# Optimization experiments

Hardware: AMD Instinct MI355X
Metric: run time of the kernel (lower is better)

The kernel has to match this reference:

```python
import jax, jax.numpy as jnp
import numpy as np

B, C, HS, WS = 4, 256, 64, 64
NK, NV, NH = 32, 32, 8
QKV = NK * NV + NK + NV  # 1088


def setup_inputs() -> dict:
    key = jax.random.key(0)
    k1, k2, k3, k4 = jax.random.split(key, 4)
    x = jax.random.normal(k1, (B, C, HS, WS), dtype=jnp.float32)
    Wqkv = jax.random.normal(k2, (NH, QKV, C), dtype=jnp.float32) * (C ** -0.5)
    Wc = jax.random.normal(k3, (C, NV * NH), dtype=jnp.float32) * ((NV * NH) ** -0.5)
    bc = jax.random.normal(k4, (C,), dtype=jnp.float32) * 0.01
    return {"x": x, "Wqkv": Wqkv, "Wc": Wc, "bc": bc}


def reference(x, Wqkv, Wc, bc):
    b, c, h, w = x.shape
    n = h * w
    xt = x.reshape(b, c, n).transpose(0, 2, 1)  # (B, N, C)
    # All heads' QKV projections in one einsum (torch loops over heads)
    qkv = jnp.einsum('bnc,hqc->bhnq', xt, Wqkv)  # (B, NH, N, QKV)
    q = qkv[..., :NK]                                            # (B,NH,N,NK)
    k = qkv[..., NK:NK + NK * NV].reshape(b, NH, n, NK, NV)      # (B,NH,N,NK,NV)
    v = qkv[..., NK + NK * NV:]                                  # (B,NH,N,NV)
    # per-pixel tiny matmul: (1xNK) @ (NKxNV) -> NV, scaled
    qk = jnp.einsum('bhnk,bhnkv->bhnv', q, k) / (NK ** 0.5)
    a = jax.nn.softmax(qk, axis=-1) * v  # (B, NH, N, NV)
    # concat heads along channel dim (head-major), then combine Linear
    a = a.transpose(0, 2, 1, 3).reshape(b, n, NH * NV)  # (B, N, NH*NV)
    out = a @ Wc.T + bc  # (B, N, C)
    return out.transpose(0, 2, 1).reshape(b, c, h, w)
```

## Files before the change

### kernel.cpp

```cpp
#include <hip/hip_runtime.h>

#define NPIX_TOTAL 16384
#define CDIM 256
#define NHEADS 8
#define QKVD 1088
#define NQKV 8704

typedef unsigned short u16;
typedef __attribute__((ext_vector_type(8))) __bf16 bf16x8;
typedef __attribute__((ext_vector_type(4))) float f32x4;
typedef __attribute__((ext_vector_type(2))) unsigned u32x2;

__device__ static inline u16 f2bf(float f) {
  union { float f; unsigned u; } x; x.f = f;
  unsigned r = x.u + 0x7fffu + ((x.u >> 16) & 1u);
  return (u16)(r >> 16);
}

__device__ static inline void gload_lds16(const void* g, void* l) {
  __builtin_amdgcn_global_load_lds((const __attribute__((address_space(1))) void*)g,
                                   (__attribute__((address_space(3))) void*)l,
                                   16, 0, 0);
}

#define WAITVM(N) asm volatile("s_waitcnt vmcnt(" #N ")" ::: "memory")
#define BARRIER() asm volatile("s_barrier" ::: "memory")

__global__ __launch_bounds__(256) void transpose_cast(const float* __restrict__ x,
                                                      u16* __restrict__ xt) {
  __shared__ float t[64][65];
  const int b = blockIdx.z;
  const float* xb = x + (size_t)b * CDIM * 4096;
  u16* ob = xt + (size_t)b * 4096 * CDIM;
  const int n0 = blockIdx.x * 64;
  const int c0 = blockIdx.y * 64;
  const int tx = threadIdx.x & 63;
  const int ty = threadIdx.x >> 6;
#pragma unroll
  for (int i = 0; i < 16; ++i)
    t[ty + i * 4][tx] = xb[(size_t)(c0 + ty + i * 4) * 4096 + n0 + tx];
  __syncthreads();
#pragma unroll
  for (int i = 0; i < 16; ++i)
    ob[(size_t)(n0 + ty + i * 4) * CDIM + c0 + tx] = f2bf(t[tx][ty + i * 4]);
}

__global__ __launch_bounds__(256) void cast_bf(const float* __restrict__ in,
                                               u16* __restrict__ out, int n) {
  const int i = (blockIdx.x * 256 + threadIdx.x) * 4;
  if (i >= n) return;
  const f32x4 v = *(const f32x4*)(in + i);
  *(unsigned*)(out + i) = (unsigned)f2bf(v.x) | ((unsigned)f2bf(v.y) << 16);
  *(unsigned*)(out + i + 2) = (unsigned)f2bf(v.z) | ((unsigned)f2bf(v.w) << 16);
}

__global__ __launch_bounds__(512, 2) void fused_qkv_attn(const u16* __restrict__ Xbf,
                                                         const u16* __restrict__ Wbf,
                                                         u16* __restrict__ Abf) {
  __shared__ u16 A_lds[128 * 256];
  __shared__ u16 B_lds[2 * 256 * 64];
  __shared__ float q_lds[128 * 32];

  const int tid = threadIdx.x;
  const int lane = tid & 63;
  const int l15 = lane & 15;
  const int hi = lane >> 4;
  const int wid = tid >> 6;
  const int wr = wid >> 2;
  const int wn = wid & 3;
  const int wm = wr * 64;

  const int head = blockIdx.x & 7;
  const int pixtile = blockIdx.x >> 3;
  const u16* Ag = Xbf + (size_t)pixtile * 128 * CDIM;
  const u16* Wh = Wbf + (size_t)head * QKVD * CDIM;

  auto stageA = [&]() {
#pragma unroll
    for (int i = 0; i < 8; ++i) {
      const int seg = wid * 8 + i;
      const int L = seg * 64 + lane;
      const int row = L >> 5;
      const int c = L & 31;
      const int cs = (c & 24) | ((c & 7) ^ (row & 7));
      gload_lds16(Ag + (size_t)row * CDIM + cs * 8, (char*)A_lds + (size_t)seg * 1024);
    }
  };
  auto stageQV = [&]() {
#pragma unroll
    for (int i = 0; i < 4; ++i) {
      const int seg = wid * 4 + i;
      const int L = seg * 64 + lane;
      const int row = L >> 5;
      const int c = L & 31;
      const int cs = (c & 24) | ((c & 7) ^ (row & 7));
      const int grow = row < 32 ? row : row + 1024;
      gload_lds16(Wh + (size_t)grow * CDIM + cs * 8, (char*)B_lds + (size_t)seg * 1024);
    }
  };
  auto stageB = [&](int buf, int t) {
#pragma unroll
    for (int i = 0; i < 4; ++i) {
      const int seg = wid * 4 + i;
      const int L = seg * 64 + lane;
      const int row = L >> 3;
      const int c8 = (L & 7) ^ (row & 7);
      const int grow = 32 + (t >> 2) * 256 + row;
      gload_lds16(Wh + (size_t)grow * CDIM + (t & 3) * 64 + c8 * 8,
                  (char*)B_lds + (size_t)buf * 32768 + (size_t)seg * 1024);
    }
  };
  auto afrag = [&](int mi, int kb, int kk2) -> bf16x8 {
    const int row = wm + mi * 16 + l15;
    const int ch = kb * 8 + ((kk2 * 4 + hi) ^ (row & 7));
    return *(const bf16x8*)(A_lds + row * 256 + ch * 8);
  };

  stageA();
  stageQV();
  WAITVM(0);
  __syncthreads();

  f32x4 accq[4] = {};
#pragma unroll
  for (int kb = 0; kb < 4; ++kb)
#pragma unroll
    for (int kk2 = 0; kk2 < 2; ++kk2) {
      const int brow = wn * 16 + l15;
      const int bch = kb * 8 + ((kk2 * 4 + hi) ^ (brow & 7));
      const bf16x8 bq = *(const bf16x8*)(B_lds + brow * 256 + bch * 8);
#pragma unroll
      for (int mi = 0; mi < 4; ++mi)
        accq[mi] = __builtin_amdgcn_mfma_f32_16x16x32_bf16(bq, afrag(mi, kb, kk2),
                                                           accq[mi], 0, 0, 0);
    }
  if (wn < 2) {
#pragma unroll
    for (int mi = 0; mi < 4; ++mi) {
      const int pix = wm + mi * 16 + l15;
      *(f32x4*)(q_lds + pix * 32 + ((wn * 4 + hi) ^ (pix & 7)) * 4) = accq[mi];
    }
  }
  __syncthreads();

  f32x4 acc[4][4] = {};
  f32x4 qkr[4][2] = {};
  stageB(0, 0);
  WAITVM(0);

#pragma unroll 1
  for (int s = 0; s < 4; ++s) {
#pragma unroll
    for (int kb = 0; kb < 4; ++kb) {
      const int t = s * 4 + kb;
      BARRIER();
      if (t < 15) stageB((t + 1) & 1, t + 1);
      const u16* bs = B_lds + (t & 1) * 16384;
#pragma unroll
      for (int kk2 = 0; kk2 < 2; ++kk2) {
        bf16x8 bfr[4], af[4];
#pragma unroll
        for (int ni = 0; ni < 4; ++ni) {
          const int row = wn * 64 + ni * 16 + l15;
          bfr[ni] = *(const bf16x8*)(bs + row * 64 + (((kk2 * 4 + hi) ^ (row & 7))) * 8);
        }
#pragma unroll
        for (int mi = 0; mi < 4; ++mi) af[mi] = afrag(mi, kb, kk2);
        __builtin_amdgcn_s_setprio(1);
#pragma unroll
        for (int mi = 0; mi < 4; ++mi)
#pragma unroll
          for (int ni = 0; ni < 4; ++ni)
            acc[mi][ni] = __builtin_amdgcn_mfma_f32_16x16x32_bf16(bfr[ni], af[mi],
                                                                  acc[mi][ni], 0, 0, 0);
        __builtin_amdgcn_s_setprio(0);
      }
      if (kb == 3) {
#pragma unroll
        for (int mi = 0; mi < 4; ++mi) {
          const int pix = wm + mi * 16 + l15;
          const float* qrow = q_lds + pix * 32;
#pragma unroll
          for (int kp = 0; kp < 2; ++kp) {
            const int k = s * 8 + wn * 2 + kp;
            const float qv_ = qrow[((k >> 2) ^ (pix & 7)) * 4 + (k & 3)];
            qkr[mi][0] += qv_ * acc[mi][kp * 2 + 0];
            qkr[mi][1] += qv_ * acc[mi][kp * 2 + 1];
          }
#pragma unroll
          for (int ni = 0; ni < 4; ++ni) acc[mi][ni] = (f32x4){0.f, 0.f, 0.f, 0.f};
        }
      }
      WAITVM(4);
    }
  }

  __syncthreads();
  float* part = (float*)B_lds;
#pragma unroll
  for (int mi = 0; mi < 4; ++mi)
#pragma unroll
    for (int par = 0; par < 2; ++par) {
      const int pix = wm + mi * 16 + l15;
      const int ch = (par * 4 + hi) ^ (pix & 7);
      *(f32x4*)(part + wn * 4096 + pix * 32 + ch * 4) = qkr[mi][par];
    }
  __syncthreads();

  const float scale = 0.17677669529663687f;
#pragma unroll
  for (int mi = 0; mi < 4; ++mi) {
    const int pix = wm + mi * 16 + l15;
    const int ch0 = (0 * 4 + hi) ^ (pix & 7);
    const int ch1 = (1 * 4 + hi) ^ (pix & 7);
    f32x4 q0 = {0.f, 0.f, 0.f, 0.f}, q1 = {0.f, 0.f, 0.f, 0.f};
#pragma unroll
    for (int w = 0; w < 4; ++w) {
      q0 += *(const f32x4*)(part + w * 4096 + pix * 32 + ch0 * 4);
      q1 += *(const f32x4*)(part + w * 4096 + pix * 32 + ch1 * 4);
    }
    q0 *= scale; q1 *= scale;
    float m = fmaxf(fmaxf(fmaxf(q0.x, q0.y), fmaxf(q0.z, q0.w)),
                    fmaxf(fmaxf(q1.x, q1.y), fmaxf(q1.z, q1.w)));
    m = fmaxf(m, __shfl_xor(m, 16));
    m = fmaxf(m, __shfl_xor(m, 32));
    f32x4 e0, e1;
    e0.x = __expf(q0.x - m); e0.y = __expf(q0.y - m);
    e0.z = __expf(q0.z - m); e0.w = __expf(q0.w - m);
    e1.x = __expf(q1.x - m); e1.y = __expf(q1.y - m);
    e1.z = __expf(q1.z - m); e1.w = __expf(q1.w - m);
    float su = e0.x + e0.y + e0.z + e0.w + e1.x + e1.y + e1.z + e1.w;
    su += __shfl_xor(su, 16);
    su += __shfl_xor(su, 32);
    if (wn >= 2) {
      const float inv = 1.0f / su;
      const f32x4 a = (wn == 2 ? e0 : e1) * (accq[mi] * inv);
      u32x2 p;
      p.x = (unsigned)f2bf(a.x) | ((unsigned)f2bf(a.y) << 16);
      p.y = (unsigned)f2bf(a.z) | ((unsigned)f2bf(a.w) << 16);
      const size_t gp = (size_t)(pixtile * 128 + pix) * 256 + head * 32 + (wn - 2) * 16 + hi * 4;
      *(u32x2*)(Abf + gp) = p;
    }
  }
}

__global__ __launch_bounds__(256, 2) void gemm_out(const u16* __restrict__ A,
                                                   const u16* __restrict__ B,
                                                   float* __restrict__ Cout,
                                                   const float* __restrict__ bias) {
  __shared__ u16 As[2][128 * 64];
  __shared__ u16 Bs[2][128 * 64];
  const int tid = threadIdx.x;
  const int lane = tid & 63;
  const int wv = tid >> 6;
  const size_t m0 = (size_t)blockIdx.y * 128;
  const size_t n0 = (size_t)blockIdx.x * 128;
  const int wm = (wv >> 1) * 64;
  const int wn = (wv & 1) * 64;
  const int frow = lane & 15;
  const int fh = lane >> 4;
  const int fsw = frow & 7;

  f32x4 acc[4][4] = {};

  auto stage = [&](int buf, int kt) {
#pragma unroll
    for (int i = 0; i < 4; ++i) {
      const int L = (i * 4 + wv) * 64 + lane;
      const int r = L >> 3;
      const int cs = (L & 7) ^ (r & 7);
      const size_t goff = (size_t)r * CDIM + kt * 64 + cs * 8;
      gload_lds16(A + m0 * CDIM + goff, (char*)As[buf] + (size_t)(i * 4 + wv) * 1024);
      gload_lds16(B + n0 * CDIM + goff, (char*)Bs[buf] + (size_t)(i * 4 + wv) * 1024);
    }
  };

  stage(0, 0);
#pragma unroll
  for (int kt = 0; kt < 4; ++kt) {
    __syncthreads();
    if (kt < 3) stage((kt + 1) & 1, kt + 1);
    const u16* as = As[kt & 1];
    const u16* bs = Bs[kt & 1];
#pragma unroll
    for (int kk2 = 0; kk2 < 2; ++kk2) {
      const int kc = (kk2 * 4 + fh) ^ fsw;
      bf16x8 af[4], bfr[4];
#pragma unroll
      for (int mi = 0; mi < 4; ++mi)
        af[mi] = *(const bf16x8*)(as + (wm + mi * 16 + frow) * 64 + kc * 8);
#pragma unroll
      for (int ni = 0; ni < 4; ++ni)
        bfr[ni] = *(const bf16x8*)(bs + (wn + ni * 16 + frow) * 64 + kc * 8);
#pragma unroll
      for (int mi = 0; mi < 4; ++mi)
#pragma unroll
        for (int ni = 0; ni < 4; ++ni)
          acc[mi][ni] =
              __builtin_amdgcn_mfma_f32_16x16x32_bf16(af[mi], bfr[ni], acc[mi][ni], 0, 0, 0);
    }
  }

#pragma unroll
  for (int mi = 0; mi < 4; ++mi)
#pragma unroll
    for (int ni = 0; ni < 4; ++ni) {
      const size_t gm = m0 + wm + mi * 16 + fh * 4;
      const size_t gn = n0 + wn + ni * 16 + frow;
      f32x4 v = acc[mi][ni];
      v += bias[gn];
      const size_t b = gm >> 12;
      const size_t pix = gm & 4095;
      *(f32x4*)(Cout + ((b << 8) + gn) * 4096 + pix) = v;
    }
}

extern "C" void kernel_launch(void* const* d_in, const int* in_sizes, int n_in,
                              void* d_out, int out_size, void* d_ws, size_t ws_size,
                              hipStream_t stream) {
  (void)in_sizes; (void)n_in; (void)out_size; (void)ws_size;
  const float* x = (const float*)d_in[0];
  const float* Wqkv = (const float*)d_in[1];
  const float* Wc = (const float*)d_in[2];
  const float* bc = (const float*)d_in[3];
  float* out = (float*)d_out;
  char* ws = (char*)d_ws;

  const size_t XBF_OFF = 0;
  const size_t WBF_OFF = 8388608;
  const size_t WCBF_OFF = 12845056;
  const size_t ABF_OFF = 12976128;
  u16* Xbf = (u16*)(ws + XBF_OFF);
  u16* Wbf = (u16*)(ws + WBF_OFF);
  u16* Wcbf = (u16*)(ws + WCBF_OFF);
  u16* Abf = (u16*)(ws + ABF_OFF);

  transpose_cast<<<dim3(64, 4, 4), 256, 0, stream>>>(x, Xbf);
  cast_bf<<<(NQKV * CDIM) / 1024, 256, 0, stream>>>(Wqkv, Wbf, NQKV * CDIM);
  cast_bf<<<(CDIM * 256) / 1024, 256, 0, stream>>>(Wc, Wcbf, CDIM * 256);

  fused_qkv_attn<<<dim3((NPIX_TOTAL / 128) * NHEADS), 512, 0, stream>>>(Xbf, Wbf, Abf);

  gemm_out<<<dim3(256 / 128, NPIX_TOTAL / 128), 256, 0, stream>>>(Abf, Wcbf, out, bc);
}
```

Before: 113.4 us.

## Load weight fragments directly from global into registers, dropping the B LDS staging

The kernel stops staging the QKV weight tiles through a double-buffered LDS buffer. Each wave now reads its B fragments straight from global memory into registers, with a two-deep register prefetch (bA/bB) in place of the barrier-synchronised LDS pipeline. The q/v weight fragments are likewise read directly into registers, and the cross-wave partial-sum scratch reuses A_lds. This removes 64KB of LDS and the per-step barriers, which may allow more blocks per CU. The cost is duplicated global/L2 traffic, since waves sharing a column tile load the same weights, plus much higher VGPR pressure with a risk of spills or exposed load latency.

```diff
diff --git a/kernel.cpp b/kernel.cpp
--- a/kernel.cpp
+++ b/kernel.cpp
@@ -22,9 +22,6 @@
                                    (__attribute__((address_space(3))) void*)l,
                                    16, 0, 0);
 }
-
-#define WAITVM(N) asm volatile("s_waitcnt vmcnt(" #N ")" ::: "memory")
-#define BARRIER() asm volatile("s_barrier" ::: "memory")
 
 __global__ __launch_bounds__(256) void transpose_cast(const float* __restrict__ x,
                                                       u16* __restrict__ xt) {
@@ -58,7 +55,6 @@
                                                          const u16* __restrict__ Wbf,
                                                          u16* __restrict__ Abf) {
   __shared__ u16 A_lds[128 * 256];
-  __shared__ u16 B_lds[2 * 256 * 64];
   __shared__ float q_lds[128 * 32];
 
   const int tid = threadIdx.x;
@@ -75,65 +71,42 @@
   const u16* Ag = Xbf + (size_t)pixtile * 128 * CDIM;
   const u16* Wh = Wbf + (size_t)head * QKVD * CDIM;
 
-  auto stageA = [&]() {
-#pragma unroll
-    for (int i = 0; i < 8; ++i) {
-      const int seg = wid * 8 + i;
-      const int L = seg * 64 + lane;
-      const int row = L >> 5;
-      const int c = L & 31;
-      const int cs = (c & 24) | ((c & 7) ^ (row & 7));
-      gload_lds16(Ag + (size_t)row * CDIM + cs * 8, (char*)A_lds + (size_t)seg * 1024);
-    }
-  };
-  auto stageQV = [&]() {
-#pragma unroll
-    for (int i = 0; i < 4; ++i) {
-      const int seg = wid * 4 + i;
-      const int L = seg * 64 + lane;
-      const int row = L >> 5;
-      const int c = L & 31;
-      const int cs = (c & 24) | ((c & 7) ^ (row & 7));
-      const int grow = row < 32 ? row : row + 1024;
-      gload_lds16(Wh + (size_t)grow * CDIM + cs * 8, (char*)B_lds + (size_t)seg * 1024);
-    }
-  };
-  auto stageB = [&](int buf, int t) {
-#pragma unroll
-    for (int i = 0; i < 4; ++i) {
-      const int seg = wid * 4 + i;
-      const int L = seg * 64 + lane;
-      const int row = L >> 3;
-      const int c8 = (L & 7) ^ (row & 7);
-      const int grow = 32 + (t >> 2) * 256 + row;
-      gload_lds16(Wh + (size_t)grow * CDIM + (t & 3) * 64 + c8 * 8,
-                  (char*)B_lds + (size_t)buf * 32768 + (size_t)seg * 1024);
-    }
-  };
+#pragma unroll
+  for (int i = 0; i < 8; ++i) {
+    const int seg = wid * 8 + i;
+    const int L = seg * 64 + lane;
+    const int row = L >> 5;
+    const int c = L & 31;
+    const int cs = (c & 24) | ((c & 7) ^ (row & 7));
+    gload_lds16(Ag + (size_t)row * CDIM + cs * 8, (char*)A_lds + (size_t)seg * 1024);
+  }
+
+  const int brow = wn * 16 + l15;
+  const u16* qvbase = Wh + (size_t)(brow < 32 ? brow : brow + 1024) * CDIM + hi * 8;
+  bf16x8 bq[4][2];
+#pragma unroll
+  for (int kb = 0; kb < 4; ++kb)
+#pragma unroll
+    for (int kk2 = 0; kk2 < 2; ++kk2)
+      bq[kb][kk2] = *(const bf16x8*)(qvbase + kb * 64 + kk2 * 32);
+
+  __syncthreads();
+
   auto afrag = [&](int mi, int kb, int kk2) -> bf16x8 {
     const int row = wm + mi * 16 + l15;
     const int ch = kb * 8 + ((kk2 * 4 + hi) ^ (row & 7));
     return *(const bf16x8*)(A_lds + row * 256 + ch * 8);
   };
 
-  stageA();
-  stageQV();
-  WAITVM(0);
-  __syncthreads();
-
   f32x4 accq[4] = {};
 #pragma unroll
   for (int kb = 0; kb < 4; ++kb)
 #pragma unroll
-    for (int kk2 = 0; kk2 < 2; ++kk2) {
-      const int brow = wn * 16 + l15;
-      const int bch = kb * 8 + ((kk2 * 4 + hi) ^ (brow & 7));
-      const bf16x8 bq = *(const bf16x8*)(B_lds + brow * 256 + bch * 8);
+    for (int kk2 = 0; kk2 < 2; ++kk2)
 #pragma unroll
       for (int mi = 0; mi < 4; ++mi)
-        accq[mi] = __builtin_amdgcn_mfma_f32_16x16x32_bf16(bq, afrag(mi, kb, kk2),
+        accq[mi] = __builtin_amdgcn_mfma_f32_16x16x32_bf16(bq[kb][kk2], afrag(mi, kb, kk2),
                                                            accq[mi], 0, 0, 0);
-    }
   if (wn < 2) {
 #pragma unroll
     for (int mi = 0; mi < 4; ++mi) {
@@ -145,58 +118,64 @@
 
   f32x4 acc[4][4] = {};
   f32x4 qkr[4][2] = {};
-  stageB(0, 0);
-  WAITVM(0);
-
-#pragma unroll 1
-  for (int s = 0; s < 4; ++s) {
-#pragma unroll
-    for (int kb = 0; kb < 4; ++kb) {
-      const int t = s * 4 + kb;
-      BARRIER();
-      if (t < 15) stageB((t + 1) & 1, t + 1);
-      const u16* bs = B_lds + (t & 1) * 16384;
-#pragma unroll
-      for (int kk2 = 0; kk2 < 2; ++kk2) {
-        bf16x8 bfr[4], af[4];
-#pragma unroll
-        for (int ni = 0; ni < 4; ++ni) {
-          const int row = wn * 64 + ni * 16 + l15;
-          bfr[ni] = *(const bf16x8*)(bs + row * 64 + (((kk2 * 4 + hi) ^ (row & 7))) * 8);
+  const u16* Bbase = Wh + (size_t)(32 + wn * 64 + l15) * CDIM + hi * 8;
+
+  auto loadB = [&](bf16x8 (&dst)[2][4], int t) {
+    const u16* p = Bbase + (size_t)(t >> 2) * 256 * CDIM + (t & 3) * 64;
+#pragma unroll
+    for (int kk2 = 0; kk2 < 2; ++kk2)
+#pragma unroll
+      for (int ni = 0; ni < 4; ++ni)
+        dst[kk2][ni] = *(const bf16x8*)(p + (size_t)ni * 16 * CDIM + kk2 * 32);
+  };
+
+  auto mstep = [&](bf16x8 (&bfr)[2][4], int t) {
+#pragma unroll
+    for (int kk2 = 0; kk2 < 2; ++kk2) {
+      bf16x8 af[4];
+#pragma unroll
+      for (int mi = 0; mi < 4; ++mi) af[mi] = afrag(mi, t & 3, kk2);
+      __builtin_amdgcn_s_setprio(1);
+#pragma unroll
+      for (int mi = 0; mi < 4; ++mi)
+#pragma unroll
+        for (int ni = 0; ni < 4; ++ni)
+          acc[mi][ni] = __builtin_amdgcn_mfma_f32_16x16x32_bf16(bfr[kk2][ni], af[mi],
+                                                                acc[mi][ni], 0, 0, 0);
+      __builtin_amdgcn_s_setprio(0);
+    }
+    if ((t & 3) == 3) {
+      const int s = t >> 2;
+#pragma unroll
+      for (int mi = 0; mi < 4; ++mi) {
+        const int pix = wm + mi * 16 + l15;
+        const float* qrow = q_lds + pix * 32;
+#pragma unroll
+        for (int kp = 0; kp < 2; ++kp) {
+          const int k = s * 8 + wn * 2 + kp;
+          const float qv_ = qrow[((k >> 2) ^ (pix & 7)) * 4 + (k & 3)];
+          qkr[mi][0] += qv_ * acc[mi][kp * 2 + 0];
+          qkr[mi][1] += qv_ * acc[mi][kp * 2 + 1];
         }
 #pragma unroll
-        for (int mi = 0; mi < 4; ++mi) af[mi] = afrag(mi, kb, kk2);
-        __builtin_amdgcn_s_setprio(1);
-#pragma unroll
-        for (int mi = 0; mi < 4; ++mi)
-#pragma unroll
-          for (int ni = 0; ni < 4; ++ni)
-            acc[mi][ni] = __builtin_amdgcn_mfma_f32_16x16x32_bf16(bfr[ni], af[mi],
-                                                                  acc[mi][ni], 0, 0, 0);
-        __builtin_amdgcn_s_setprio(0);
+        for (int ni = 0; ni < 4; ++ni) acc[mi][ni] = (f32x4){0.f, 0.f, 0.f, 0.f};
       }
-      if (kb == 3) {
-#pragma unroll
-        for (int mi = 0; mi < 4; ++mi) {
-          const int pix = wm + mi * 16 + l15;
-          const float* qrow = q_lds + pix * 32;
-#pragma unroll
-          for (int kp = 0; kp < 2; ++kp) {
-            const int k = s * 8 + wn * 2 + kp;
-            const float qv_ = qrow[((k >> 2) ^ (pix & 7)) * 4 + (k & 3)];
-            qkr[mi][0] += qv_ * acc[mi][kp * 2 + 0];
-            qkr[mi][1] += qv_ * acc[mi][kp * 2 + 1];
-          }
-#pragma unroll
-          for (int ni = 0; ni < 4; ++ni) acc[mi][ni] = (f32x4){0.f, 0.f, 0.f, 0.f};
-        }
-      }
-      WAITVM(4);
-    }
-  }
-
-  __syncthreads();
-  float* part = (float*)B_lds;
+    }
+  };
+
+  bf16x8 bA[2][4], bB[2][4];
+  loadB(bA, 0);
+  loadB(bB, 1);
+#pragma unroll
+  for (int tt = 0; tt < 16; tt += 2) {
+    mstep(bA, tt);
+    if (tt + 2 < 16) loadB(bA, tt + 2);
+    mstep(bB, tt + 1);
+    if (tt + 3 < 16) loadB(bB, tt + 3);
+  }
+
+  __syncthreads();
+  float* part = (float*)A_lds;
 #pragma unroll
   for (int mi = 0; mi < 4; ++mi)
 #pragma unroll
@@ -211,8 +190,8 @@
 #pragma unroll
   for (int mi = 0; mi < 4; ++mi) {
     const int pix = wm + mi * 16 + l15;
-    const int ch0 = (0 * 4 + hi) ^ (pix & 7);
-    const int ch1 = (1 * 4 + hi) ^ (pix & 7);
+    const int ch0 = hi ^ (pix & 7);
+    const int ch1 = (4 + hi) ^ (pix & 7);
     f32x4 q0 = {0.f, 0.f, 0.f, 0.f}, q1 = {0.f, 0.f, 0.f, 0.f};
 #pragma unroll
     for (int w = 0; w < 4; ++w) {
```

Result: slower. 166.9 us (+47.2%).

## Restructure K-projection loop into 4-deep ring of smaller B tiles

Applied to the files above, without the earlier changes.

Replaces the double-buffered 256x64 weight tiles with a 4-slot ring of 128x64 tiles, prefetched three steps ahead, and loops over 32 steps instead of 16. Each wave now owns 32 output columns, which halves the accumulator registers, and the q-weighted reduction is folded into every step. A fragments are loaded only once per kb. The cross-wave partial sums reuse A_lds instead of the B buffer. The aim is deeper latency hiding and lower register pressure, at the cost of more barriers and more frequent q_lds reads.

```diff
diff --git a/kernel.cpp b/kernel.cpp
--- a/kernel.cpp
+++ b/kernel.cpp
@@ -58,7 +58,7 @@
                                                          const u16* __restrict__ Wbf,
                                                          u16* __restrict__ Abf) {
   __shared__ u16 A_lds[128 * 256];
-  __shared__ u16 B_lds[2 * 256 * 64];
+  __shared__ u16 Bring[4][128 * 64];
   __shared__ float q_lds[128 * 32];
 
   const int tid = threadIdx.x;
@@ -75,60 +75,42 @@
   const u16* Ag = Xbf + (size_t)pixtile * 128 * CDIM;
   const u16* Wh = Wbf + (size_t)head * QKVD * CDIM;
 
-  auto stageA = [&]() {
-#pragma unroll
-    for (int i = 0; i < 8; ++i) {
-      const int seg = wid * 8 + i;
-      const int L = seg * 64 + lane;
-      const int row = L >> 5;
-      const int c = L & 31;
-      const int cs = (c & 24) | ((c & 7) ^ (row & 7));
-      gload_lds16(Ag + (size_t)row * CDIM + cs * 8, (char*)A_lds + (size_t)seg * 1024);
-    }
-  };
-  auto stageQV = [&]() {
-#pragma unroll
-    for (int i = 0; i < 4; ++i) {
-      const int seg = wid * 4 + i;
-      const int L = seg * 64 + lane;
-      const int row = L >> 5;
-      const int c = L & 31;
-      const int cs = (c & 24) | ((c & 7) ^ (row & 7));
-      const int grow = row < 32 ? row : row + 1024;
-      gload_lds16(Wh + (size_t)grow * CDIM + cs * 8, (char*)B_lds + (size_t)seg * 1024);
-    }
-  };
-  auto stageB = [&](int buf, int t) {
-#pragma unroll
-    for (int i = 0; i < 4; ++i) {
-      const int seg = wid * 4 + i;
-      const int L = seg * 64 + lane;
-      const int row = L >> 3;
-      const int c8 = (L & 7) ^ (row & 7);
-      const int grow = 32 + (t >> 2) * 256 + row;
-      gload_lds16(Wh + (size_t)grow * CDIM + (t & 3) * 64 + c8 * 8,
-                  (char*)B_lds + (size_t)buf * 32768 + (size_t)seg * 1024);
-    }
-  };
+#pragma unroll
+  for (int i = 0; i < 8; ++i) {
+    const int seg = wid * 8 + i;
+    const int L = seg * 64 + lane;
+    const int row = L >> 5;
+    const int c = L & 31;
+    const int cs = (c & 24) | ((c & 7) ^ (row & 7));
+    gload_lds16(Ag + (size_t)row * CDIM + cs * 8, (char*)A_lds + (size_t)seg * 1024);
+  }
+#pragma unroll
+  for (int i = 0; i < 4; ++i) {
+    const int seg = wid * 4 + i;
+    const int L = seg * 64 + lane;
+    const int row = L >> 5;
+    const int c = L & 31;
+    const int cs = (c & 24) | ((c & 7) ^ (row & 7));
+    const int grow = row < 32 ? row : row + 1024;
+    gload_lds16(Wh + (size_t)grow * CDIM + cs * 8, (char*)&Bring[0][0] + (size_t)seg * 1024);
+  }
+  WAITVM(0);
+  __syncthreads();
+
   auto afrag = [&](int mi, int kb, int kk2) -> bf16x8 {
     const int row = wm + mi * 16 + l15;
     const int ch = kb * 8 + ((kk2 * 4 + hi) ^ (row & 7));
     return *(const bf16x8*)(A_lds + row * 256 + ch * 8);
   };
 
-  stageA();
-  stageQV();
-  WAITVM(0);
-  __syncthreads();
-
   f32x4 accq[4] = {};
+  const int brow = wn * 16 + l15;
 #pragma unroll
   for (int kb = 0; kb < 4; ++kb)
 #pragma unroll
     for (int kk2 = 0; kk2 < 2; ++kk2) {
-      const int brow = wn * 16 + l15;
       const int bch = kb * 8 + ((kk2 * 4 + hi) ^ (brow & 7));
-      const bf16x8 bq = *(const bf16x8*)(B_lds + brow * 256 + bch * 8);
+      const bf16x8 bq = *(const bf16x8*)(&Bring[0][0] + brow * 256 + bch * 8);
 #pragma unroll
       for (int mi = 0; mi < 4; ++mi)
         accq[mi] = __builtin_amdgcn_mfma_f32_16x16x32_bf16(bq, afrag(mi, kb, kk2),
@@ -143,60 +125,75 @@
   }
   __syncthreads();
 
-  f32x4 acc[4][4] = {};
+  f32x4 acc[4][2] = {};
   f32x4 qkr[4][2] = {};
-  stageB(0, 0);
-  WAITVM(0);
-
+  bf16x8 afc[4][2];
+
+  auto stage = [&](int t) {
+    const int kb = t >> 3, sh = t & 7;
+    u16* dst = &Bring[t & 3][0];
+#pragma unroll
+    for (int i = 0; i < 2; ++i) {
+      const int L = i * 512 + wid * 64 + lane;
+      const int row = L >> 3;
+      const int c8 = (L & 7) ^ (row & 7);
+      gload_lds16(Wh + (size_t)(32 + sh * 128 + row) * CDIM + kb * 64 + c8 * 8,
+                  (char*)dst + (size_t)(i * 512 + wid * 64) * 16);
+    }
+  };
+
+  auto step = [&](int t) {
+    const int sh = t & 7;
+    if (sh == 0) {
+      const int kb = t >> 3;
+#pragma unroll
+      for (int mi = 0; mi < 4; ++mi)
+#pragma unroll
+        for (int kk2 = 0; kk2 < 2; ++kk2) afc[mi][kk2] = afrag(mi, kb, kk2);
+    }
+    const u16* bs = &Bring[t & 3][0];
+    bf16x8 bfr[2][2];
+#pragma unroll
+    for (int ni = 0; ni < 2; ++ni)
+#pragma unroll
+      for (int kk2 = 0; kk2 < 2; ++kk2) {
+        const int rr = wn * 32 + ni * 16 + l15;
+        bfr[ni][kk2] = *(const bf16x8*)(bs + rr * 64 + (((kk2 * 4 + hi) ^ (rr & 7))) * 8);
+      }
+    __builtin_amdgcn_s_setprio(1);
+#pragma unroll
+    for (int mi = 0; mi < 4; ++mi)
+#pragma unroll
+      for (int ni = 0; ni < 2; ++ni)
+#pragma unroll
+        for (int kk2 = 0; kk2 < 2; ++kk2)
+          acc[mi][ni] = __builtin_amdgcn_mfma_f32_16x16x32_bf16(bfr[ni][kk2], afc[mi][kk2],
+                                                                acc[mi][ni], 0, 0, 0);
+    __builtin_amdgcn_s_setprio(0);
+#pragma unroll
+    for (int mi = 0; mi < 4; ++mi) {
+      const int pix = wm + mi * 16 + l15;
+      const float qv_ = q_lds[pix * 32 + (sh ^ (pix & 7)) * 4 + wn];
+      qkr[mi][0] += qv_ * acc[mi][0];
+      qkr[mi][1] += qv_ * acc[mi][1];
+      acc[mi][0] = (f32x4){0.f, 0.f, 0.f, 0.f};
+      acc[mi][1] = (f32x4){0.f, 0.f, 0.f, 0.f};
+    }
+  };
+
+  stage(0); stage(1); stage(2);
 #pragma unroll 1
-  for (int s = 0; s < 4; ++s) {
-#pragma unroll
-    for (int kb = 0; kb < 4; ++kb) {
-      const int t = s * 4 + kb;
-      BARRIER();
-      if (t < 15) stageB((t + 1) & 1, t + 1);
-      const u16* bs = B_lds + (t & 1) * 16384;
-#pragma unroll
-      for (int kk2 = 0; kk2 < 2; ++kk2) {
-        bf16x8 bfr[4], af[4];
-#pragma unroll
-        for (int ni = 0; ni < 4; ++ni) {
-          const int row = wn * 64 + ni * 16 + l15;
-          bfr[ni] = *(const bf16x8*)(bs + row * 64 + (((kk2 * 4 + hi) ^ (row & 7))) * 8);
-        }
-#pragma unroll
-        for (int mi = 0; mi < 4; ++mi) af[mi] = afrag(mi, kb, kk2);
-        __builtin_amdgcn_s_setprio(1);
-#pragma unroll
-        for (int mi = 0; mi < 4; ++mi)
-#pragma unroll
-          for (int ni = 0; ni < 4; ++ni)
-            acc[mi][ni] = __builtin_amdgcn_mfma_f32_16x16x32_bf16(bfr[ni], af[mi],
-                                                                  acc[mi][ni], 0, 0, 0);
-        __builtin_amdgcn_s_setprio(0);
-      }
-      if (kb == 3) {
-#pragma unroll
-        for (int mi = 0; mi < 4; ++mi) {
-          const int pix = wm + mi * 16 + l15;
-          const float* qrow = q_lds + pix * 32;
-#pragma unroll
-          for (int kp = 0; kp < 2; ++kp) {
-            const int k = s * 8 + wn * 2 + kp;
-            const float qv_ = qrow[((k >> 2) ^ (pix & 7)) * 4 + (k & 3)];
-            qkr[mi][0] += qv_ * acc[mi][kp * 2 + 0];
-            qkr[mi][1] += qv_ * acc[mi][kp * 2 + 1];
-          }
-#pragma unroll
-          for (int ni = 0; ni < 4; ++ni) acc[mi][ni] = (f32x4){0.f, 0.f, 0.f, 0.f};
-        }
-      }
-      WAITVM(4);
-    }
-  }
-
-  __syncthreads();
-  float* part = (float*)B_lds;
+  for (int t = 0; t < 30; ++t) {
+    WAITVM(4);
+    BARRIER();
+    if (t < 29) stage(t + 3);
+    step(t);
+  }
+  WAITVM(2); BARRIER(); step(30);
+  WAITVM(0); BARRIER(); step(31);
+
+  __syncthreads();
+  float* part = (float*)A_lds;
 #pragma unroll
   for (int mi = 0; mi < 4; ++mi)
 #pragma unroll
@@ -211,8 +208,8 @@
 #pragma unroll
   for (int mi = 0; mi < 4; ++mi) {
     const int pix = wm + mi * 16 + l15;
-    const int ch0 = (0 * 4 + hi) ^ (pix & 7);
-    const int ch1 = (1 * 4 + hi) ^ (pix & 7);
+    const int ch0 = hi ^ (pix & 7);
+    const int ch1 = (4 + hi) ^ (pix & 7);
     f32x4 q0 = {0.f, 0.f, 0.f, 0.f}, q1 = {0.f, 0.f, 0.f, 0.f};
 #pragma unroll
     for (int w = 0; w < 4; ++w) {
```

New measurement: 135.0 us. +19.1%, slower.

## Give each wave a private B ring to drop block barriers from the main loop

Applied to the files above, without the earlier changes.

Replaces the block-shared double-buffered B tile with per-wave private LDS buffers. Each wave streams only its own 64-row slice, in 32-wide K steps, through a depth-2 ring synchronised by vmcnt waits alone. This removes the per-step s_barrier in the main loop. The cost is that waves sharing a column slice now load the same weights twice, and there are twice as many loop iterations. The reduction scratch moves from B_lds to A_lds.

```diff
diff --git a/kernel.cpp b/kernel.cpp
--- a/kernel.cpp
+++ b/kernel.cpp
@@ -24,7 +24,6 @@
 }
 
 #define WAITVM(N) asm volatile("s_waitcnt vmcnt(" #N ")" ::: "memory")
-#define BARRIER() asm volatile("s_barrier" ::: "memory")
 
 __global__ __launch_bounds__(256) void transpose_cast(const float* __restrict__ x,
                                                       u16* __restrict__ xt) {
@@ -58,7 +57,7 @@
                                                          const u16* __restrict__ Wbf,
                                                          u16* __restrict__ Abf) {
   __shared__ u16 A_lds[128 * 256];
-  __shared__ u16 B_lds[2 * 256 * 64];
+  __shared__ u16 B_lds[8][2][2048];
   __shared__ float q_lds[128 * 32];
 
   const int tid = threadIdx.x;
@@ -74,66 +73,51 @@
   const int pixtile = blockIdx.x >> 3;
   const u16* Ag = Xbf + (size_t)pixtile * 128 * CDIM;
   const u16* Wh = Wbf + (size_t)head * QKVD * CDIM;
-
-  auto stageA = [&]() {
-#pragma unroll
-    for (int i = 0; i < 8; ++i) {
-      const int seg = wid * 8 + i;
-      const int L = seg * 64 + lane;
-      const int row = L >> 5;
-      const int c = L & 31;
-      const int cs = (c & 24) | ((c & 7) ^ (row & 7));
-      gload_lds16(Ag + (size_t)row * CDIM + cs * 8, (char*)A_lds + (size_t)seg * 1024);
-    }
-  };
-  auto stageQV = [&]() {
-#pragma unroll
-    for (int i = 0; i < 4; ++i) {
-      const int seg = wid * 4 + i;
-      const int L = seg * 64 + lane;
-      const int row = L >> 5;
-      const int c = L & 31;
-      const int cs = (c & 24) | ((c & 7) ^ (row & 7));
-      const int grow = row < 32 ? row : row + 1024;
-      gload_lds16(Wh + (size_t)grow * CDIM + cs * 8, (char*)B_lds + (size_t)seg * 1024);
-    }
-  };
-  auto stageB = [&](int buf, int t) {
-#pragma unroll
-    for (int i = 0; i < 4; ++i) {
-      const int seg = wid * 4 + i;
-      const int L = seg * 64 + lane;
-      const int row = L >> 3;
-      const int c8 = (L & 7) ^ (row & 7);
-      const int grow = 32 + (t >> 2) * 256 + row;
-      gload_lds16(Wh + (size_t)grow * CDIM + (t & 3) * 64 + c8 * 8,
-                  (char*)B_lds + (size_t)buf * 32768 + (size_t)seg * 1024);
-    }
-  };
+  u16* ring = &B_lds[0][0][0];
+
+#pragma unroll
+  for (int i = 0; i < 8; ++i) {
+    const int seg = wid * 8 + i;
+    const int L = seg * 64 + lane;
+    const int row = L >> 5;
+    const int c = L & 31;
+    const int cs = (c & 24) | ((c & 7) ^ (row & 7));
+    gload_lds16(Ag + (size_t)row * CDIM + cs * 8, (char*)A_lds + (size_t)seg * 1024);
+  }
+#pragma unroll
+  for (int i = 0; i < 4; ++i) {
+    const int seg = wid * 4 + i;
+    const int L = seg * 64 + lane;
+    const int row = L >> 5;
+    const int c = L & 31;
+    const int cs = (c & 24) | ((c & 7) ^ (row & 7));
+    const int grow = row < 32 ? row : row + 1024;
+    gload_lds16(Wh + (size_t)grow * CDIM + cs * 8, (char*)ring + (size_t)seg * 1024);
+  }
+  WAITVM(0);
+  __syncthreads();
+
   auto afrag = [&](int mi, int kb, int kk2) -> bf16x8 {
     const int row = wm + mi * 16 + l15;
     const int ch = kb * 8 + ((kk2 * 4 + hi) ^ (row & 7));
     return *(const bf16x8*)(A_lds + row * 256 + ch * 8);
   };
 
-  stageA();
-  stageQV();
-  WAITVM(0);
-  __syncthreads();
-
   f32x4 accq[4] = {};
-#pragma unroll
-  for (int kb = 0; kb < 4; ++kb)
-#pragma unroll
-    for (int kk2 = 0; kk2 < 2; ++kk2) {
-      const int brow = wn * 16 + l15;
-      const int bch = kb * 8 + ((kk2 * 4 + hi) ^ (brow & 7));
-      const bf16x8 bq = *(const bf16x8*)(B_lds + brow * 256 + bch * 8);
-#pragma unroll
-      for (int mi = 0; mi < 4; ++mi)
-        accq[mi] = __builtin_amdgcn_mfma_f32_16x16x32_bf16(bq, afrag(mi, kb, kk2),
-                                                           accq[mi], 0, 0, 0);
-    }
+  {
+    const int brow = wn * 16 + l15;
+#pragma unroll
+    for (int kb = 0; kb < 4; ++kb)
+#pragma unroll
+      for (int kk2 = 0; kk2 < 2; ++kk2) {
+        const int bch = kb * 8 + ((kk2 * 4 + hi) ^ (brow & 7));
+        const bf16x8 bq = *(const bf16x8*)(ring + brow * 256 + bch * 8);
+#pragma unroll
+        for (int mi = 0; mi < 4; ++mi)
+          accq[mi] = __builtin_amdgcn_mfma_f32_16x16x32_bf16(bq, afrag(mi, kb, kk2),
+                                                             accq[mi], 0, 0, 0);
+      }
+  }
   if (wn < 2) {
 #pragma unroll
     for (int mi = 0; mi < 4; ++mi) {
@@ -145,58 +129,69 @@
 
   f32x4 acc[4][4] = {};
   f32x4 qkr[4][2] = {};
-  stageB(0, 0);
-  WAITVM(0);
-
+
+  auto stage = [&](int t) {
+    const int s = t >> 3, ks = t & 7;
+    char* dst = (char*)&B_lds[wid][t & 1][0];
+    const u16* src = Wh + (size_t)(32 + s * 256 + wn * 64) * CDIM + ks * 32;
+#pragma unroll
+    for (int i = 0; i < 4; ++i) {
+      const int row = i * 16 + (lane >> 2);
+      const int cs = (lane & 3) ^ (row & 3);
+      gload_lds16(src + (size_t)row * CDIM + cs * 8, dst + i * 1024);
+    }
+  };
+
+  auto mstep = [&](int t) {
+    const int ks = t & 7;
+    const u16* bs = &B_lds[wid][t & 1][0];
+    bf16x8 bfr[4], af[4];
+#pragma unroll
+    for (int ni = 0; ni < 4; ++ni) {
+      const int row = ni * 16 + l15;
+      bfr[ni] = *(const bf16x8*)(bs + row * 32 + (hi ^ (row & 3)) * 8);
+    }
+#pragma unroll
+    for (int mi = 0; mi < 4; ++mi) af[mi] = afrag(mi, ks >> 1, ks & 1);
+    __builtin_amdgcn_s_setprio(1);
+#pragma unroll
+    for (int mi = 0; mi < 4; ++mi)
+#pragma unroll
+      for (int ni = 0; ni < 4; ++ni)
+        acc[mi][ni] = __builtin_amdgcn_mfma_f32_16x16x32_bf16(bfr[ni], af[mi],
+                                                              acc[mi][ni], 0, 0, 0);
+    __builtin_amdgcn_s_setprio(0);
+    if (ks == 7) {
+      const int s = t >> 3;
+#pragma unroll
+      for (int mi = 0; mi < 4; ++mi) {
+        const int pix = wm + mi * 16 + l15;
+        const float* qrow = q_lds + pix * 32;
+#pragma unroll
+        for (int kp = 0; kp < 2; ++kp) {
+          const int k = s * 8 + wn * 2 + kp;
+          const float qv_ = qrow[((k >> 2) ^ (pix & 7)) * 4 + (k & 3)];
+          qkr[mi][0] += qv_ * acc[mi][kp * 2 + 0];
+          qkr[mi][1] += qv_ * acc[mi][kp * 2 + 1];
+        }
+#pragma unroll
+        for (int ni = 0; ni < 4; ++ni) acc[mi][ni] = (f32x4){0.f, 0.f, 0.f, 0.f};
+      }
+    }
+  };
+
+  stage(0);
+  stage(1);
 #pragma unroll 1
-  for (int s = 0; s < 4; ++s) {
-#pragma unroll
-    for (int kb = 0; kb < 4; ++kb) {
-      const int t = s * 4 + kb;
-      BARRIER();
-      if (t < 15) stageB((t + 1) & 1, t + 1);
-      const u16* bs = B_lds + (t & 1) * 16384;
-#pragma unroll
-      for (int kk2 = 0; kk2 < 2; ++kk2) {
-        bf16x8 bfr[4], af[4];
-#pragma unroll
-        for (int ni = 0; ni < 4; ++ni) {
-          const int row = wn * 64 + ni * 16 + l15;
-          bfr[ni] = *(const bf16x8*)(bs + row * 64 + (((kk2 * 4 + hi) ^ (row & 7))) * 8);
-        }
-#pragma unroll
-        for (int mi = 0; mi < 4; ++mi) af[mi] = afrag(mi, kb, kk2);
-        __builtin_amdgcn_s_setprio(1);
-#pragma unroll
-        for (int mi = 0; mi < 4; ++mi)
-#pragma unroll
-          for (int ni = 0; ni < 4; ++ni)
-            acc[mi][ni] = __builtin_amdgcn_mfma_f32_16x16x32_bf16(bfr[ni], af[mi],
-                                                                  acc[mi][ni], 0, 0, 0);
-        __builtin_amdgcn_s_setprio(0);
-      }
-      if (kb == 3) {
-#pragma unroll
-        for (int mi = 0; mi < 4; ++mi) {
-          const int pix = wm + mi * 16 + l15;
-          const float* qrow = q_lds + pix * 32;
-#pragma unroll
-          for (int kp = 0; kp < 2; ++kp) {
-            const int k = s * 8 + wn * 2 + kp;
-            const float qv_ = qrow[((k >> 2) ^ (pix & 7)) * 4 + (k & 3)];
-            qkr[mi][0] += qv_ * acc[mi][kp * 2 + 0];
-            qkr[mi][1] += qv_ * acc[mi][kp * 2 + 1];
-          }
-#pragma unroll
-          for (int ni = 0; ni < 4; ++ni) acc[mi][ni] = (f32x4){0.f, 0.f, 0.f, 0.f};
-        }
-      }
-      WAITVM(4);
-    }
-  }
-
-  __syncthreads();
-  float* part = (float*)B_lds;
+  for (int t = 0; t < 32; ++t) {
+    if (t == 31) { WAITVM(0); } else { WAITVM(4); }
+    mstep(t);
+    __builtin_amdgcn_sched_barrier(0);
+    if (t < 30) stage(t + 2);
+  }
+
+  __syncthreads();
+  float* part = (float*)A_lds;
 #pragma unroll
   for (int mi = 0; mi < 4; ++mi)
 #pragma unroll
@@ -211,8 +206,8 @@
 #pragma unroll
   for (int mi = 0; mi < 4; ++mi) {
     const int pix = wm + mi * 16 + l15;
-    const int ch0 = (0 * 4 + hi) ^ (pix & 7);
-    const int ch1 = (1 * 4 + hi) ^ (pix & 7);
+    const int ch0 = hi ^ (pix & 7);
+    const int ch1 = (4 + hi) ^ (pix & 7);
     f32x4 q0 = {0.f, 0.f, 0.f, 0.f}, q1 = {0.f, 0.f, 0.f, 0.f};
 #pragma unroll
     for (int w = 0; w < 4; ++w) {
```

Measured after the change: 121.5 us. +7.2%, slower.
